# Kernel optimization log

Measured on AMD Instinct MI355X. Metric: run time of the kernel, lower is better.

Reference implementation:

```python
import math
import jax, jax.numpy as jnp
import numpy as np

B, T, M, D = 65536, 20, 4, 4   # batch, timesteps, regions, d_reg
L, H, FF = 3, 2, 16            # layers, heads, dim_feedforward
S = M + 1                      # seq_len with cls token
TAU = 10000.0


def setup_inputs() -> dict:
    key = jax.random.key(0)
    ks = jax.random.split(key, 8)

    def w(k, shape, std=0.1):
        return jax.random.normal(k, shape, dtype=jnp.float32) * std

    return {
        "regional_states": jax.random.normal(ks[0], (B, T, M, D), dtype=jnp.float32),
        "cls_token": w(ks[1], (1, 1, D), 0.02),
        # stacked per-layer params (layer axis first)
        "Wqkv": w(ks[2], (L, 3 * D, D)),   # nn.MultiheadAttention in_proj_weight
        "bqkv": jnp.zeros((L, 3 * D), jnp.float32),
        "Wo": w(ks[3], (L, D, D)),          # out_proj weight
        "bo": jnp.zeros((L, D), jnp.float32),
        "W1": w(ks[4], (L, FF, D)),         # linear1 weight (torch layout: out, in)
        "b1": jnp.zeros((L, FF), jnp.float32),
        "W2": w(ks[5], (L, D, FF)),         # linear2 weight
        "b2": jnp.zeros((L, D), jnp.float32),
    }


def _positional_encoding():
    # PE(pos,2i)=sin(pos/tau^(2i/D)), PE(pos,2i+1)=cos(...)
    pos = jnp.arange(S, dtype=jnp.float32)[:, None]            # (S,1)
    div = jnp.exp(jnp.arange(0, D, 2, dtype=jnp.float32) * (-math.log(TAU) / D))
    pe = jnp.zeros((S, D), jnp.float32)
    pe = pe.at[:, 0::2].set(jnp.sin(pos * div))
    pe = pe.at[:, 1::2].set(jnp.cos(pos * div))
    return pe  # (S, D)


def _layer(x, Wqkv, bqkv, Wo, bo, W1, b1, W2, b2):
    # x: (N, S, D). Dropout is identity (eval mode).
    N, Sq, Dm = x.shape
    hd = Dm // H
    qkv = x @ Wqkv.T + bqkv                     # (N, S, 3D)
    q, k, v = jnp.split(qkv, 3, axis=-1)

    def heads(t):
        return t.reshape(N, Sq, H, hd).transpose(0, 2, 1, 3)  # (N, H, S, hd)

    q, k, v = heads(q), heads(k), heads(v)
    scores = jnp.einsum("nhqd,nhkd->nhqk", q, k) / math.sqrt(hd)
    attn = jax.nn.softmax(scores, axis=-1)
    o = jnp.einsum("nhqk,nhkd->nhqd", attn, v)
    o = o.transpose(0, 2, 1, 3).reshape(N, Sq, Dm)
    attn_out = o @ Wo.T + bo
    x = x + attn_out                            # residual (no norm)
    ff = jax.nn.relu(x @ W1.T + b1) @ W2.T + b2
    return x + ff


def reference(regional_states, cls_token, Wqkv, bqkv, Wo, bo, W1, b1, W2, b2):
    Bq, Tq, Mq, Dq = regional_states.shape
    N = Bq * Tq
    x = regional_states.reshape(N, Mq, Dq)
    cls = jnp.broadcast_to(cls_token, (N, 1, Dq))
    x = jnp.concatenate([cls, x], axis=1)       # (N, S, D)
    x = x + _positional_encoding()[None, :, :]
    for i in range(L):
        x = _layer(x, Wqkv[i], bqkv[i], Wo[i], bo[i], W1[i], b1[i], W2[i], b2[i])
    F_g = x[:, 0, :].reshape(Bq, Tq, Dq)
    subregion_seq = x[:, 1:, :].reshape(Bq, Tq, Mq * Dq)
    return (F_g, subregion_seq)
```

## Files before the change

kernel.cpp:

```cpp
#include <hip/hip_runtime.h>


typedef _Float16 h2 __attribute__((ext_vector_type(2)));

enum {
  WF_CLS  = 0,
  WF_BQKV = 4,
  WF_BO   = 40,
  WF_B2   = 52,
  H_B1    = 64,
  H_QKV   = 88,
  H_WO    = 160,
  H_W1    = 184,
  H_W2    = 280,
  WF_FLAG = 376,
  WF_TOTAL = 377
};

__device__ __forceinline__ float bf2f(unsigned short u) {
  unsigned int x = ((unsigned int)u) << 16;
  float f;
  __builtin_memcpy(&f, &x, 4);
  return f;
}

__device__ __forceinline__ bool is_bf16_packed(const unsigned int* w) {
  int pass = 0;
#pragma unroll
  for (int i = 0; i < 16; ++i) {
    unsigned int lo = w[i] & 0xFFFFu;
    unsigned int e = (lo >> 7) & 0xFFu;
    if (lo == 0u || (e >= 90u && e <= 140u)) ++pass;
  }
  return pass >= 15;
}

__device__ __forceinline__ float dot2(h2 a, h2 b, float c) {
#if __has_builtin(__builtin_amdgcn_fdot2)
  return __builtin_amdgcn_fdot2(a, b, c, false);
#else
  return fmaf((float)a.x, (float)b.x, fmaf((float)a.y, (float)b.y, c));
#endif
}

__device__ __forceinline__ h2 pk(float a, float b) {
  auto t = __builtin_amdgcn_cvt_pkrtz(a, b);
  h2 r;
  __builtin_memcpy(&r, &t, sizeof(r));
  return r;
}

__device__ __forceinline__ h2 relu2(h2 a) {
  h2 z = {(_Float16)0.0f, (_Float16)0.0f};
#if __has_builtin(__builtin_elementwise_max)
  return __builtin_elementwise_max(a, z);
#else
  h2 r;
  r.x = a.x > z.x ? a.x : z.x;
  r.y = a.y > z.y ? a.y : z.y;
  return r;
#endif
}

__device__ __forceinline__ float fexp2(float x) {
#if __has_builtin(__builtin_amdgcn_exp2f)
  return __builtin_amdgcn_exp2f(x);
#else
  return __builtin_exp2f(x);
#endif
}

__global__ void mpt_prep(const void* __restrict__ cls,
                         const void* __restrict__ Wqkv,
                         const void* __restrict__ bqkv,
                         const void* __restrict__ Wo,
                         const void* __restrict__ bo,
                         const void* __restrict__ W1,
                         const void* __restrict__ b1,
                         const void* __restrict__ W2,
                         const void* __restrict__ b2,
                         const void* __restrict__ xin,
                         float* __restrict__ wf) {
  const bool wbf = is_bf16_packed((const unsigned int*)Wqkv);
  const bool xbf = is_bf16_packed((const unsigned int*)xin);
  const float FS = 1.44269504088896341f * 0.70710678118654752f;

  for (int w = threadIdx.x; w < WF_TOTAL; w += 256) {
    if (w == WF_FLAG) { ((int*)wf)[w] = xbf ? 0 : 1; continue; }

    auto g = [&](const void* src, int idx) -> float {
      return wbf ? bf2f(((const unsigned short*)src)[idx])
                 : ((const float*)src)[idx];
    };

    if (w < H_B1) {
      float val;
      if (w < WF_BQKV) {
        val = g(cls, w) + ((w & 1) ? 1.0f : 0.0f);
      } else if (w < WF_BO) {
        int t = w - WF_BQKV;
        val = g(bqkv, t);
        int j = t % 12;
        if (j >= 4 && j < 8) val *= FS;
      } else if (w < WF_B2) {
        val = g(bo, w - WF_BO);
      } else {
        val = g(b2, w - WF_B2);
      }
      wf[w] = val;
    } else {
      if (w < H_QKV) {
        int t = w - H_B1, l = t / 8, p = t % 8;
        int base = l * 16 + 2 * p;
        ((h2*)wf)[w] = pk(g(b1, base), g(b1, base + 1));
      } else if (w < H_WO) {
        int t = w - H_QKV, l = t / 24, j = (t % 24) / 2, p = t & 1;
        int base = l * 48 + j * 4 + p * 2;
        float s = (j >= 4 && j < 8) ? FS : 1.0f;
        ((h2*)wf)[w] = pk(g(Wqkv, base) * s, g(Wqkv, base + 1) * s);
      } else if (w < H_W1) {
        int t = w - H_WO, l = t / 8, i = (t % 8) / 2, p = t & 1;
        int base = l * 16 + i * 4 + p * 2;
        ((h2*)wf)[w] = pk(g(Wo, base), g(Wo, base + 1));
      } else if (w < H_W2) {
        int t = w - H_W1, l = t / 32, p = (t % 32) / 4, d = t % 4;
        int base = l * 64 + 8 * p + d;
        ((h2*)wf)[w] = pk(g(W1, base), g(W1, base + 4));
      } else {
        int t = w - H_W2, l = t / 32, i = (t % 32) / 8, p = t % 8;
        int base = l * 64 + i * 16 + p * 2;
        ((h2*)wf)[w] = pk(g(W2, base), g(W2, base + 1));
      }
    }
  }
}

__global__ __launch_bounds__(256) void mpt_main(
    const void* __restrict__ xin,
    const float* __restrict__ wf,
    float* __restrict__ out,
    int N) {
  const int n = blockIdx.x * 256 + threadIdx.x;
  if (n >= N) return;

  const int xf32 = ((const int*)wf)[WF_FLAG];
  const h2* hw = (const h2*)wf;

  const float pe[4][4] = {
    { 0.8414709848078965f, 0.5403023058681398f, 0.0099998333341667f, 0.9999500004166653f },
    { 0.9092974268256817f,-0.4161468365471424f, 0.0199986666933331f, 0.9998000066665778f },
    { 0.1411200080598672f,-0.9899924966004454f, 0.0299955002024957f, 0.9995500337489875f },
    {-0.7568024953079283f,-0.6536436208636119f, 0.0399893341866342f, 0.9992001066609779f }
  };

  float raw[16];
  if (xf32) {
    const float4* pf = reinterpret_cast<const float4*>((const float*)xin + (size_t)n * 16);
#pragma unroll
    for (int r = 0; r < 4; ++r) {
      float4 t = pf[r];
      raw[r * 4 + 0] = t.x; raw[r * 4 + 1] = t.y;
      raw[r * 4 + 2] = t.z; raw[r * 4 + 3] = t.w;
    }
  } else {
    struct alignas(16) U8 { unsigned short v[8]; };
    const U8* p = reinterpret_cast<const U8*>((const unsigned short*)xin + (size_t)n * 16);
    U8 a0 = p[0], a1 = p[1];
#pragma unroll
    for (int j = 0; j < 8; ++j) {
      raw[j]     = bf2f(a0.v[j]);
      raw[8 + j] = bf2f(a1.v[j]);
    }
  }

  float x[5][4];
#pragma unroll
  for (int d = 0; d < 4; ++d) x[0][d] = wf[WF_CLS + d];
#pragma unroll
  for (int r = 0; r < 4; ++r)
#pragma unroll
    for (int d = 0; d < 4; ++d) x[1 + r][d] = raw[r * 4 + d] + pe[r][d];

#pragma unroll
  for (int l = 0; l < 3; ++l) {
    const float* bq  = wf + WF_BQKV + l * 12;
    const float* bo  = wf + WF_BO   + l * 4;
    const float* b2  = wf + WF_B2   + l * 4;
    const h2* hb1  = hw + H_B1  + l * 8;
    const h2* hq   = hw + H_QKV + l * 24;
    const h2* hwo  = hw + H_WO  + l * 8;
    const h2* hw1p = hw + H_W1  + l * 32;
    const h2* hw2  = hw + H_W2  + l * 32;

    h2 xh[5][2];
#pragma unroll
    for (int s = 0; s < 5; ++s) {
      xh[s][0] = pk(x[s][0], x[s][1]);
      xh[s][1] = pk(x[s][2], x[s][3]);
    }

    float q[5][4], k[5][4], v[5][4];
#pragma unroll
    for (int s = 0; s < 5; ++s) {
#pragma unroll
      for (int j = 0; j < 12; ++j) {
        float a = dot2(xh[s][0], hq[j * 2],
                       dot2(xh[s][1], hq[j * 2 + 1], bq[j]));
        if (j < 4)      q[s][j] = a;
        else if (j < 8) k[s][j - 4] = a;
        else            v[s][j - 8] = a;
      }
    }

    float o[5][4];
#pragma unroll
    for (int h = 0; h < 2; ++h) {
      const int d0 = 2 * h, d1 = 2 * h + 1;
      h2 qh[5], kh[5];
#pragma unroll
      for (int s = 0; s < 5; ++s) {
        qh[s] = pk(q[s][d0], q[s][d1]);
        kh[s] = pk(k[s][d0], k[s][d1]);
      }
#pragma unroll
      for (int si = 0; si < 5; ++si) {
        float e[5], den = 0.f;
#pragma unroll
        for (int sj = 0; sj < 5; ++sj) {
          e[sj] = fexp2(dot2(qh[si], kh[sj], 0.0f));
          den += e[sj];
        }
        float inv = __builtin_amdgcn_rcpf(den);
        float o0 = 0.f, o1 = 0.f;
#pragma unroll
        for (int sj = 0; sj < 5; ++sj) {
          o0 = fmaf(e[sj], v[sj][d0], o0);
          o1 = fmaf(e[sj], v[sj][d1], o1);
        }
        o[si][d0] = o0 * inv;
        o[si][d1] = o1 * inv;
      }
    }

#pragma unroll
    for (int s = 0; s < 5; ++s) {
      h2 oh0 = pk(o[s][0], o[s][1]), oh1 = pk(o[s][2], o[s][3]);
      float nx[4];
#pragma unroll
      for (int i = 0; i < 4; ++i)
        nx[i] = dot2(oh0, hwo[i * 2],
                     dot2(oh1, hwo[i * 2 + 1], x[s][i] + bo[i]));

      h2 xb[4];
      float acc[4];
#pragma unroll
      for (int d = 0; d < 4; ++d) xb[d] = pk(nx[d], nx[d]);
#pragma unroll
      for (int i = 0; i < 4; ++i) acc[i] = b2[i];
#pragma unroll
      for (int p = 0; p < 8; ++p) {
        h2 hc = hb1[p];
#pragma unroll
        for (int d = 0; d < 4; ++d) hc = xb[d] * hw1p[p * 4 + d] + hc;
        h2 hh = relu2(hc);
#pragma unroll
        for (int i = 0; i < 4; ++i) acc[i] = dot2(hh, hw2[i * 8 + p], acc[i]);
      }
#pragma unroll
      for (int i = 0; i < 4; ++i) x[s][i] = nx[i] + acc[i];
    }
  }

  *reinterpret_cast<float4*>(out + (size_t)n * 4) =
      make_float4(x[0][0], x[0][1], x[0][2], x[0][3]);
  float* sub = out + (size_t)N * 4 + (size_t)n * 16;
#pragma unroll
  for (int r = 0; r < 4; ++r)
    *reinterpret_cast<float4*>(sub + r * 4) =
        make_float4(x[1 + r][0], x[1 + r][1], x[1 + r][2], x[1 + r][3]);
}

extern "C" void kernel_launch(void* const* d_in, const int* in_sizes, int n_in,
                              void* d_out, int out_size, void* d_ws, size_t ws_size,
                              hipStream_t stream) {
  float* wf = (float*)d_ws;

  mpt_prep<<<1, 256, 0, stream>>>(
      d_in[1], d_in[2], d_in[3], d_in[4], d_in[5],
      d_in[6], d_in[7], d_in[8], d_in[9],
      d_in[0],
      wf);

  const int N = in_sizes[0] / 16;
  mpt_main<<<(N + 255) / 256, 256, 0, stream>>>(
      d_in[0], wf, (float*)d_out, N);
}
```

Measured before the change: 263.6 us.

## Precompute layer-0 CLS QKV, fold out-proj bias, pack softmax into dot2

Layer 0's CLS-token QKV does not depend on the input, so it is now computed once during weight preprocessing and read from the weight buffer. The out-projection bias is folded into the FFN biases (b1 += W1·bo, b2 += bo), which removes per-token adds. The softmax denominator and value weighting are restructured to use packed fp16 dot2 operations, and the attention output is kept in packed form. These cut per-token ALU work in exchange for more fp16 rounding of the exp weights and slightly more setup work.

```diff
diff --git a/kernel.cpp b/kernel.cpp
--- a/kernel.cpp
+++ b/kernel.cpp
@@ -13,8 +13,9 @@
   H_WO    = 160,
   H_W1    = 184,
   H_W2    = 280,
-  WF_FLAG = 376,
-  WF_TOTAL = 377
+  WF_QKV0 = 376,
+  WF_FLAG = 388,
+  WF_TOTAL = 389
 };
 
 __device__ __forceinline__ float bf2f(unsigned short u) {
@@ -93,6 +94,19 @@
                  : ((const float*)src)[idx];
     };
 
+    if (w >= WF_QKV0) {
+      int j = w - WF_QKV0;
+      float acc = g(bqkv, j);
+#pragma unroll
+      for (int d = 0; d < 4; ++d) {
+        float xc = g(cls, d) + ((d & 1) ? 1.0f : 0.0f);
+        acc = fmaf(g(Wqkv, j * 4 + d), xc, acc);
+      }
+      if (j >= 4 && j < 8) acc *= FS;
+      wf[w] = acc;
+      continue;
+    }
+
     if (w < H_B1) {
       float val;
       if (w < WF_BQKV) {
@@ -105,14 +119,22 @@
       } else if (w < WF_B2) {
         val = g(bo, w - WF_BO);
       } else {
-        val = g(b2, w - WF_B2);
+        int t = w - WF_B2;
+        val = g(b2, t) + g(bo, t);
       }
       wf[w] = val;
     } else {
       if (w < H_QKV) {
         int t = w - H_B1, l = t / 8, p = t % 8;
-        int base = l * 16 + 2 * p;
-        ((h2*)wf)[w] = pk(g(b1, base), g(b1, base + 1));
+        int f0 = 2 * p, f1 = 2 * p + 1;
+        float v0 = g(b1, l * 16 + f0), v1 = g(b1, l * 16 + f1);
+#pragma unroll
+        for (int d = 0; d < 4; ++d) {
+          float bod = g(bo, l * 4 + d);
+          v0 = fmaf(g(W1, l * 64 + f0 * 4 + d), bod, v0);
+          v1 = fmaf(g(W1, l * 64 + f1 * 4 + d), bod, v1);
+        }
+        ((h2*)wf)[w] = pk(v0, v1);
       } else if (w < H_WO) {
         int t = w - H_QKV, l = t / 24, j = (t % 24) / 2, p = t & 1;
         int base = l * 48 + j * 4 + p * 2;
@@ -181,10 +203,11 @@
 #pragma unroll
     for (int d = 0; d < 4; ++d) x[1 + r][d] = raw[r * 4 + d] + pe[r][d];
 
+  const h2 one2 = pk(1.0f, 1.0f);
+
 #pragma unroll
   for (int l = 0; l < 3; ++l) {
     const float* bq  = wf + WF_BQKV + l * 12;
-    const float* bo  = wf + WF_BO   + l * 4;
     const float* b2  = wf + WF_B2   + l * 4;
     const h2* hb1  = hw + H_B1  + l * 8;
     const h2* hq   = hw + H_QKV + l * 24;
@@ -195,6 +218,7 @@
     h2 xh[5][2];
 #pragma unroll
     for (int s = 0; s < 5; ++s) {
+      if (l == 0 && s == 0) continue;
       xh[s][0] = pk(x[s][0], x[s][1]);
       xh[s][1] = pk(x[s][2], x[s][3]);
     }
@@ -202,6 +226,15 @@
     float q[5][4], k[5][4], v[5][4];
 #pragma unroll
     for (int s = 0; s < 5; ++s) {
+      if (l == 0 && s == 0) {
+#pragma unroll
+        for (int j = 0; j < 4; ++j) {
+          q[0][j] = wf[WF_QKV0 + j];
+          k[0][j] = wf[WF_QKV0 + 4 + j];
+          v[0][j] = wf[WF_QKV0 + 8 + j];
+        }
+        continue;
+      }
 #pragma unroll
       for (int j = 0; j < 12; ++j) {
         float a = dot2(xh[s][0], hq[j * 2],
@@ -212,7 +245,7 @@
       }
     }
 
-    float o[5][4];
+    h2 oh[5][2];
 #pragma unroll
     for (int h = 0; h < 2; ++h) {
       const int d0 = 2 * h, d1 = 2 * h + 1;
@@ -222,34 +255,32 @@
         qh[s] = pk(q[s][d0], q[s][d1]);
         kh[s] = pk(k[s][d0], k[s][d1]);
       }
+      h2 vp0[2], vp1[2];
+      vp0[0] = pk(v[0][d0], v[1][d0]); vp0[1] = pk(v[2][d0], v[3][d0]);
+      vp1[0] = pk(v[0][d1], v[1][d1]); vp1[1] = pk(v[2][d1], v[3][d1]);
 #pragma unroll
       for (int si = 0; si < 5; ++si) {
-        float e[5], den = 0.f;
-#pragma unroll
-        for (int sj = 0; sj < 5; ++sj) {
-          e[sj] = fexp2(dot2(qh[si], kh[sj], 0.0f));
-          den += e[sj];
-        }
+        float e0 = fexp2(dot2(qh[si], kh[0], 0.0f));
+        float e1 = fexp2(dot2(qh[si], kh[1], 0.0f));
+        float e2 = fexp2(dot2(qh[si], kh[2], 0.0f));
+        float e3 = fexp2(dot2(qh[si], kh[3], 0.0f));
+        float e4 = fexp2(dot2(qh[si], kh[4], 0.0f));
+        h2 ep0 = pk(e0, e1), ep1 = pk(e2, e3);
+        float den = dot2(ep0, one2, dot2(ep1, one2, e4));
         float inv = __builtin_amdgcn_rcpf(den);
-        float o0 = 0.f, o1 = 0.f;
-#pragma unroll
-        for (int sj = 0; sj < 5; ++sj) {
-          o0 = fmaf(e[sj], v[sj][d0], o0);
-          o1 = fmaf(e[sj], v[sj][d1], o1);
-        }
-        o[si][d0] = o0 * inv;
-        o[si][d1] = o1 * inv;
+        float a0 = dot2(ep0, vp0[0], dot2(ep1, vp0[1], e4 * v[4][d0]));
+        float a1 = dot2(ep0, vp1[0], dot2(ep1, vp1[1], e4 * v[4][d1]));
+        oh[si][h] = pk(a0 * inv, a1 * inv);
       }
     }
 
 #pragma unroll
     for (int s = 0; s < 5; ++s) {
-      h2 oh0 = pk(o[s][0], o[s][1]), oh1 = pk(o[s][2], o[s][3]);
       float nx[4];
 #pragma unroll
       for (int i = 0; i < 4; ++i)
-        nx[i] = dot2(oh0, hwo[i * 2],
-                     dot2(oh1, hwo[i * 2 + 1], x[s][i] + bo[i]));
+        nx[i] = dot2(oh[s][0], hwo[i * 2],
+                     dot2(oh[s][1], hwo[i * 2 + 1], x[s][i]));
 
       h2 xb[4];
       float acc[4];
```

New measurement: 254.3 us (median of 2 runs). -3.5%, faster.
